# Kernel optimization log

Hardware: AMD Instinct MI355X
Metric: run time of the kernel (lower is better)

## Reference

```python
import jax, jax.numpy as jnp
import numpy as np

EMBED_DIM = 1024
N_HEADS = 16
HEAD_DIM = EMBED_DIM // N_HEADS


def setup_inputs() -> dict:
    key = jax.random.key(0)
    k1, k2, k3 = jax.random.split(key, 3)
    B, T, D = 2, 2048, EMBED_DIM
    x = jax.random.normal(k1, (B, T, D), dtype=jnp.float32)
    # torch nn.Linear weights: (out_features, in_features); y = x @ W.T
    scale = 1.0 / np.sqrt(D)
    qkv_w = jax.random.uniform(k2, (3 * D, D), dtype=jnp.float32, minval=-scale, maxval=scale)
    out_w = jax.random.uniform(k3, (D, D), dtype=jnp.float32, minval=-scale, maxval=scale)
    return {"x": x, "qkv_w": qkv_w, "out_w": out_w}


def reference(x, qkv_w, out_w):
    B, T, D = x.shape
    H, hd = N_HEADS, HEAD_DIM
    qkv = jnp.einsum('btd,ed->bte', x, qkv_w)  # (B,T,3D)
    qkv = qkv.reshape(B, T, 3, H, hd)
    q = jnp.transpose(qkv[:, :, 0], (0, 2, 1, 3))  # (B,H,T,hd)
    k = jnp.transpose(qkv[:, :, 1], (0, 2, 1, 3))
    v = jnp.transpose(qkv[:, :, 2], (0, 2, 1, 3))
    scores = jnp.einsum('bhtd,bhsd->bhts', q, k) / np.sqrt(hd).astype(np.float32)
    causal = jnp.tril(jnp.ones((T, T), dtype=bool))  # True = keep
    scores = jnp.where(causal[None, None], scores, -jnp.inf)
    probs = jax.nn.softmax(scores, axis=-1)
    out = jnp.einsum('bhts,bhsd->bhtd', probs, v)
    out = jnp.transpose(out, (0, 2, 1, 3)).reshape(B, T, D)
    return jnp.einsum('btd,ed->bte', out, out_w)
```

## Files before the change

### kernel.cpp

```cpp
#include <hip/hip_runtime.h>
#include <stdint.h>

typedef __bf16 bf16;
typedef __attribute__((ext_vector_type(8))) __bf16 bf16x8;
typedef __attribute__((ext_vector_type(4))) __bf16 bf16x4;
typedef __attribute__((ext_vector_type(4))) float f32x4;

#define AS1 __attribute__((address_space(1)))
#define AS3 __attribute__((address_space(3)))

__device__ __forceinline__ void async16(const void* g, void* l) {
  __builtin_amdgcn_global_load_lds((AS1 uint32_t*)(g), (AS3 uint32_t*)(l), 16, 0, 0);
}

__device__ __forceinline__ f32x4 mfma_bf16(bf16x8 a, bf16x8 b, f32x4 c) {
  return __builtin_amdgcn_mfma_f32_16x16x32_bf16(a, b, c, 0, 0, 0);
}

__device__ __forceinline__ uint32_t pack_bf16(float a, float b) {
  union { bf16 h[2]; uint32_t u; } u;
  u.h[0] = (bf16)a; u.h[1] = (bf16)b;
  return u.u;
}

__global__ __launch_bounds__(256) void cast_all_kernel(
    const float* __restrict__ x, const float* __restrict__ w1,
    const float* __restrict__ w2, bf16* __restrict__ xb,
    bf16* __restrict__ w1b, bf16* __restrict__ w2b) {
  const int bid = blockIdx.x;
  const float* src;
  bf16* dst;
  int base;
  if (bid < 4096) { src = x;  dst = xb;  base = bid; }
  else if (bid < 7168) { src = w1; dst = w1b; base = bid - 4096; }
  else { src = w2; dst = w2b; base = bid - 7168; }
  const int i = (base * 256 + threadIdx.x) * 4;
  const float4 v = *(const float4*)(src + i);
  bf16x4 o;
  o[0] = (bf16)v.x; o[1] = (bf16)v.y; o[2] = (bf16)v.z; o[3] = (bf16)v.w;
  *(bf16x4*)(dst + i) = o;
}

__global__ __launch_bounds__(256) void gemm_qkv_kernel(
    const bf16* __restrict__ A, const bf16* __restrict__ W,
    bf16* __restrict__ QK, bf16* __restrict__ VT) {
  constexpr int K = 1024;
  __shared__ __align__(16) bf16 sm[2 * 128 * 32];
  const int tid = threadIdx.x;
  const int w = tid >> 6, lane = tid & 63;
  const int m0 = blockIdx.x * 128, n0 = blockIdx.y * 128;
  const int wm = (w >> 1) * 64, wn = (w & 1) * 64;
  const int lrow = lane & 15, quad = lane >> 4;
  const int lk = quad * 8;
  f32x4 acc[4][4] = {};

  for (int k0 = 0; k0 < K; k0 += 32) {
#pragma unroll
    for (int i = 0; i < 4; ++i) {
      const int c = tid + 256 * i;
      const bf16* src = (c < 512)
          ? (A + (size_t)(m0 + (c >> 2)) * K + k0 + (c & 3) * 8)
          : (W + (size_t)(n0 + ((c - 512) >> 2)) * K + k0 + (c & 3) * 8);
      async16(src, sm + (w * 64 + i * 256) * 8);
    }
    __syncthreads();
    bf16x8 af[4], bfr[4];
#pragma unroll
    for (int mi = 0; mi < 4; ++mi)
      af[mi] = *(const bf16x8*)&sm[(wm + mi * 16 + lrow) * 32 + lk];
#pragma unroll
    for (int ni = 0; ni < 4; ++ni)
      bfr[ni] = *(const bf16x8*)&sm[128 * 32 + (wn + ni * 16 + lrow) * 32 + lk];
#pragma unroll
    for (int mi = 0; mi < 4; ++mi)
#pragma unroll
      for (int ni = 0; ni < 4; ++ni)
        acc[mi][ni] = mfma_bf16(af[mi], bfr[ni], acc[mi][ni]);
    __syncthreads();
  }

  bf16* s2 = sm;
  const bool isV = (n0 >= 2048);
  const int bb = m0 >> 11;
  const int mt = m0 & 2047;
  if (!isV) {
#pragma unroll
    for (int c = 0; c < 2; ++c) {
      if ((w >> 1) == c) {
#pragma unroll
        for (int mi = 0; mi < 4; ++mi)
#pragma unroll
          for (int ni = 0; ni < 4; ++ni) {
            const int nr = wn + ni * 16 + lrow;
#pragma unroll
            for (int r = 0; r < 4; ++r)
              s2[(mi * 16 + quad * 4 + r) * 128 + nr] = (bf16)acc[mi][ni][r];
          }
      }
      __syncthreads();
#pragma unroll
      for (int p = 0; p < 4; ++p) {
        const int row = p * 16 + (tid >> 4);
        const int colc = (tid & 15) * 8;
        const bf16x8 v = *(const bf16x8*)&s2[row * 128 + colc];
        *(bf16x8*)(QK + (size_t)(m0 + c * 64 + row) * 2048 + n0 + colc) = v;
      }
      __syncthreads();
    }
  } else {
#pragma unroll
    for (int c = 0; c < 2; ++c) {
      if ((w & 1) == c) {
#pragma unroll
        for (int mi = 0; mi < 4; ++mi)
#pragma unroll
          for (int ni = 0; ni < 4; ++ni) {
            const int nl = ni * 16 + lrow;
            bf16x4 pk4;
#pragma unroll
            for (int r = 0; r < 4; ++r) pk4[r] = (bf16)acc[mi][ni][r];
            *(bf16x4*)&s2[nl * 128 + wm + mi * 16 + quad * 4] = pk4;
          }
      }
      __syncthreads();
#pragma unroll
      for (int p = 0; p < 4; ++p) {
        const int row = p * 16 + (tid >> 4);
        const int colc = (tid & 15) * 8;
        const bf16x8 v = *(const bf16x8*)&s2[row * 128 + colc];
        const int vtrow = bb * 1024 + (n0 - 2048) + c * 64 + row;
        *(bf16x8*)(VT + (size_t)vtrow * 2048 + mt + colc) = v;
      }
      __syncthreads();
    }
  }
}

__global__ __launch_bounds__(128) void attn_kernel(
    const bf16* __restrict__ QK, const bf16* __restrict__ VT,
    bf16* __restrict__ AO) {
  __shared__ __align__(16) bf16 sK[2][64 * 64];
  __shared__ __align__(16) bf16 sV[2][64 * 64];
  const int bh = blockIdx.x;
  const int qt = 31 - blockIdx.y;
  const int b = bh >> 4, h = bh & 15;
  const int tid = threadIdx.x, w = tid >> 6, lane = tid & 63;
  const int q0 = qt * 64;
  const int col = lane & 15, quad = lane >> 4;
  const bf16* Qb = QK + (size_t)b * 2048 * 2048 + h * 64;
  const bf16* Kb = Qb + 1024;
  const bf16* Vb = VT + (size_t)bh * 64 * 2048;
  const float NEG_INF = -__builtin_inff();
  constexpr float QSCALE = 0.18033688011112042f;
  constexpr float FMX = 16.0f;

  int qrow[2];
  bf16x8 qf[2][2];
#pragma unroll
  for (int qtile = 0; qtile < 2; ++qtile) {
    qrow[qtile] = q0 + w * 32 + qtile * 16 + col;
#pragma unroll
    for (int kk = 0; kk < 2; ++kk) {
      bf16x8 v = *(const bf16x8*)(Qb + (size_t)qrow[qtile] * 2048 + kk * 32 + quad * 8);
#pragma unroll
      for (int e = 0; e < 8; ++e) v[e] = (bf16)((float)v[e] * QSCALE);
      qf[qtile][kk] = v;
    }
  }

  auto stage = [&](int buf, int s0) {
#pragma unroll
    for (int i = 0; i < 4; ++i) {
      const int L = tid + 128 * i;
      const int row = L >> 3;
      const int ch = (L & 7) ^ (row & 7);
      async16(Kb + (size_t)(s0 + row) * 2048 + ch * 8, &sK[buf][L * 8]);
    }
#pragma unroll
    for (int i = 0; i < 4; ++i) {
      const int L = tid + 128 * i;
      const int row = L >> 3;
      const int ch = (L & 7) ^ (row & 7);
      async16(Vb + (size_t)row * 2048 + s0 + ch * 8, &sV[buf][L * 8]);
    }
  };

  int srow[4];
#pragma unroll
  for (int m = 0; m < 4; ++m)
    srow[m] = 32 * (m & 1) + (col >> 2) * 8 + 4 * (m >> 1) + (col & 3);

  f32x4 accO[4][2] = {};
  float l_part[2] = {0.f, 0.f};

  stage(0, 0);

  auto body = [&](int kt, bool masked) {
    const int s0 = kt * 64;
    const bf16* kbuf = sK[kt & 1];
    const bf16* vbuf = sV[kt & 1];

    f32x4 st[2][4] = {};
#pragma unroll
    for (int kk = 0; kk < 2; ++kk) {
      bf16x8 kf[4];
#pragma unroll
      for (int m = 0; m < 4; ++m)
        kf[m] = *(const bf16x8*)&kbuf[srow[m] * 64 + (((kk * 4 + quad) ^ (srow[m] & 7)) * 8)];
#pragma unroll
      for (int m = 0; m < 4; ++m)
#pragma unroll
        for (int qtile = 0; qtile < 2; ++qtile)
          st[qtile][m] = mfma_bf16(kf[m], qf[qtile][kk], st[qtile][m]);
    }

    if (masked) {
#pragma unroll
      for (int qtile = 0; qtile < 2; ++qtile)
#pragma unroll
        for (int m = 0; m < 4; ++m) {
          const int kvb = s0 + 32 * (m & 1) + quad * 8 + 4 * (m >> 1);
#pragma unroll
          for (int r = 0; r < 4; ++r)
            st[qtile][m][r] = (kvb + r <= qrow[qtile]) ? st[qtile][m][r] : NEG_INF;
        }
    }

    uint32_t pk[2][4][2];
#pragma unroll
    for (int qtile = 0; qtile < 2; ++qtile) {
      float rs = 0.f;
#pragma unroll
      for (int m = 0; m < 4; ++m) {
        const float p0 = __builtin_amdgcn_exp2f(st[qtile][m][0] - FMX);
        const float p1 = __builtin_amdgcn_exp2f(st[qtile][m][1] - FMX);
        const float p2 = __builtin_amdgcn_exp2f(st[qtile][m][2] - FMX);
        const float p3 = __builtin_amdgcn_exp2f(st[qtile][m][3] - FMX);
        rs += (p0 + p1) + (p2 + p3);
        pk[qtile][m][0] = pack_bf16(p0, p1);
        pk[qtile][m][1] = pack_bf16(p2, p3);
      }
      l_part[qtile] += rs;
    }

#pragma unroll
    for (int kk = 0; kk < 2; ++kk) {
      bf16x8 vf[4];
#pragma unroll
      for (int d = 0; d < 4; ++d) {
        const int row = d * 16 + col;
        vf[d] = *(const bf16x8*)&vbuf[row * 64 + (((kk * 4 + quad) ^ (row & 7)) * 8)];
      }
#pragma unroll
      for (int qtile = 0; qtile < 2; ++qtile) {
        union { uint32_t u[4]; bf16x8 v; } f;
        f.u[0] = pk[qtile][kk][0];
        f.u[1] = pk[qtile][kk][1];
        f.u[2] = pk[qtile][2 + kk][0];
        f.u[3] = pk[qtile][2 + kk][1];
#pragma unroll
        for (int d = 0; d < 4; ++d)
          accO[d][qtile] = mfma_bf16(vf[d], f.v, accO[d][qtile]);
      }
    }
  };

  for (int kt = 0; kt < qt; ++kt) {
    __syncthreads();
    stage((kt + 1) & 1, (kt + 1) * 64);
    body(kt, false);
  }
  __syncthreads();
  body(qt, true);

  bf16* Ob = AO + (size_t)b * 2048 * 1024 + h * 64;
#pragma unroll
  for (int qtile = 0; qtile < 2; ++qtile) {
    float rs = l_part[qtile];
    rs += __shfl_xor(rs, 16);
    rs += __shfl_xor(rs, 32);
    const float inv = 1.0f / rs;
#pragma unroll
    for (int d = 0; d < 4; ++d) {
      bf16x4 o;
#pragma unroll
      for (int r = 0; r < 4; ++r) o[r] = (bf16)(accO[d][qtile][r] * inv);
      *(bf16x4*)(Ob + (size_t)qrow[qtile] * 1024 + d * 16 + quad * 4) = o;
    }
  }
}

__global__ __launch_bounds__(256) void gemm_out_kernel(
    const bf16* __restrict__ A, const bf16* __restrict__ W,
    float* __restrict__ C) {
  constexpr int K = 1024;
  __shared__ __align__(16) bf16 sm[2 * 128 * 32];
  const int tid = threadIdx.x;
  const int w = tid >> 6, lane = tid & 63;
  const int m0 = blockIdx.x * 128, n0 = blockIdx.y * 128;
  const int wm = (w >> 1) * 64, wn = (w & 1) * 64;
  const int lrow = lane & 15, lk = (lane >> 4) * 8;
  f32x4 acc[4][4] = {};

  for (int k0 = 0; k0 < K; k0 += 32) {
#pragma unroll
    for (int i = 0; i < 4; ++i) {
      const int c = tid + 256 * i;
      const bf16* src = (c < 512)
          ? (A + (size_t)(m0 + (c >> 2)) * K + k0 + (c & 3) * 8)
          : (W + (size_t)(n0 + ((c - 512) >> 2)) * K + k0 + (c & 3) * 8);
      async16(src, sm + (w * 64 + i * 256) * 8);
    }
    __syncthreads();
    bf16x8 af[4], bfr[4];
#pragma unroll
    for (int mi = 0; mi < 4; ++mi)
      af[mi] = *(const bf16x8*)&sm[(wm + mi * 16 + lrow) * 32 + lk];
#pragma unroll
    for (int ni = 0; ni < 4; ++ni)
      bfr[ni] = *(const bf16x8*)&sm[128 * 32 + (wn + ni * 16 + lrow) * 32 + lk];
#pragma unroll
    for (int mi = 0; mi < 4; ++mi)
#pragma unroll
      for (int ni = 0; ni < 4; ++ni)
        acc[mi][ni] = mfma_bf16(af[mi], bfr[ni], acc[mi][ni]);
    __syncthreads();
  }

#pragma unroll
  for (int mi = 0; mi < 4; ++mi)
#pragma unroll
    for (int ni = 0; ni < 4; ++ni) {
      const int n = n0 + wn + ni * 16 + lrow;
#pragma unroll
      for (int r = 0; r < 4; ++r) {
        const int m = m0 + wm + mi * 16 + (lane >> 4) * 4 + r;
        C[(size_t)m * 1024 + n] = acc[mi][ni][r];
      }
    }
}

extern "C" void kernel_launch(void* const* d_in, const int* in_sizes, int n_in,
                              void* d_out, int out_size, void* d_ws, size_t ws_size,
                              hipStream_t stream) {
  const float* x     = (const float*)d_in[0];
  const float* qkv_w = (const float*)d_in[1];
  const float* out_w = (const float*)d_in[2];
  float* out = (float*)d_out;

  char* ws = (char*)d_ws;
  bf16* xb    = (bf16*)(ws);
  bf16* aob   = (bf16*)(ws);
  bf16* wqkvb = (bf16*)(ws + 8u * 1024 * 1024);
  bf16* wob   = (bf16*)(ws + 14u * 1024 * 1024);
  bf16* qkb   = (bf16*)(ws + 16u * 1024 * 1024);
  bf16* vtb   = (bf16*)(ws + 32u * 1024 * 1024);

  cast_all_kernel<<<8192, 256, 0, stream>>>(x, qkv_w, out_w, xb, wqkvb, wob);
  gemm_qkv_kernel<<<dim3(32, 24), 256, 0, stream>>>(xb, wqkvb, qkb, vtb);
  attn_kernel<<<dim3(32, 32), 128, 0, stream>>>(qkb, vtb, aob);
  gemm_out_kernel<<<dim3(32, 8), 256, 0, stream>>>(aob, wob, out);
}
```

Baseline: 183.7 us.

## Split KV tiles across warp pairs in attention and reduce partials via LDS

Doubles attention block size to four warps. Each pair of warps handles the same query rows and takes alternate KV tiles, with both tiles staged into LDS together. Partial output accumulators and row sums are combined through shared memory before normalization. This raises per-block parallelism and shortens the serial KV loop, at the cost of losing prefetch/compute overlap and adding extra barriers and a final reduction.

```diff
diff --git a/kernel.cpp b/kernel.cpp
--- a/kernel.cpp
+++ b/kernel.cpp
@@ -136,7 +136,7 @@
   }
 }
 
-__global__ __launch_bounds__(128) void attn_kernel(
+__global__ __launch_bounds__(256) void attn_kernel(
     const bf16* __restrict__ QK, const bf16* __restrict__ VT,
     bf16* __restrict__ AO) {
   __shared__ __align__(16) bf16 sK[2][64 * 64];
@@ -145,6 +145,7 @@
   const int qt = 31 - blockIdx.y;
   const int b = bh >> 4, h = bh & 15;
   const int tid = threadIdx.x, w = tid >> 6, lane = tid & 63;
+  const int qhalf = w >> 1, parity = w & 1;
   const int q0 = qt * 64;
   const int col = lane & 15, quad = lane >> 4;
   const bf16* Qb = QK + (size_t)b * 2048 * 2048 + h * 64;
@@ -158,7 +159,7 @@
   bf16x8 qf[2][2];
 #pragma unroll
   for (int qtile = 0; qtile < 2; ++qtile) {
-    qrow[qtile] = q0 + w * 32 + qtile * 16 + col;
+    qrow[qtile] = q0 + qhalf * 32 + qtile * 16 + col;
 #pragma unroll
     for (int kk = 0; kk < 2; ++kk) {
       bf16x8 v = *(const bf16x8*)(Qb + (size_t)qrow[qtile] * 2048 + kk * 32 + quad * 8);
@@ -168,20 +169,22 @@
     }
   }
 
-  auto stage = [&](int buf, int s0) {
+  auto stage = [&](int s0) {
 #pragma unroll
     for (int i = 0; i < 4; ++i) {
-      const int L = tid + 128 * i;
-      const int row = L >> 3;
-      const int ch = (L & 7) ^ (row & 7);
-      async16(Kb + (size_t)(s0 + row) * 2048 + ch * 8, &sK[buf][L * 8]);
+      const int L = tid + 256 * i;
+      const int buf = L >> 9, Lr = L & 511;
+      const int row = Lr >> 3;
+      const int ch = (Lr & 7) ^ (row & 7);
+      async16(Kb + (size_t)(s0 + buf * 64 + row) * 2048 + ch * 8, &sK[0][L * 8]);
     }
 #pragma unroll
     for (int i = 0; i < 4; ++i) {
-      const int L = tid + 128 * i;
-      const int row = L >> 3;
-      const int ch = (L & 7) ^ (row & 7);
-      async16(Vb + (size_t)row * 2048 + s0 + ch * 8, &sV[buf][L * 8]);
+      const int L = tid + 256 * i;
+      const int buf = L >> 9, Lr = L & 511;
+      const int d = Lr >> 3;
+      const int ch = (Lr & 7) ^ (d & 7);
+      async16(Vb + (size_t)d * 2048 + s0 + buf * 64 + ch * 8, &sV[0][L * 8]);
     }
   };
 
@@ -193,12 +196,10 @@
   f32x4 accO[4][2] = {};
   float l_part[2] = {0.f, 0.f};
 
-  stage(0, 0);
-
   auto body = [&](int kt, bool masked) {
     const int s0 = kt * 64;
-    const bf16* kbuf = sK[kt & 1];
-    const bf16* vbuf = sV[kt & 1];
+    const bf16* kbuf = &sK[0][parity * 4096];
+    const bf16* vbuf = &sV[0][parity * 4096];
 
     f32x4 st[2][4] = {};
 #pragma unroll
@@ -265,27 +266,54 @@
     }
   };
 
-  for (int kt = 0; kt < qt; ++kt) {
-    __syncthreads();
-    stage((kt + 1) & 1, (kt + 1) * 64);
-    body(kt, false);
+  const int npairs = (qt >> 1) + 1;
+  for (int j = 0; j < npairs; ++j) {
+    stage(j * 128);
+    __syncthreads();
+    const int kt = 2 * j + parity;
+    if (kt <= qt) body(kt, kt == qt);
+    __syncthreads();
+  }
+
+  float* scrO = (float*)sK;
+  float* scrL = (float*)sV;
+  if (parity == 1) {
+    const int base = qhalf * 2048;
+#pragma unroll
+    for (int d = 0; d < 4; ++d)
+#pragma unroll
+      for (int qtile = 0; qtile < 2; ++qtile)
+#pragma unroll
+        for (int r = 0; r < 4; ++r)
+          scrO[base + ((d * 2 + qtile) * 4 + r) * 64 + lane] = accO[d][qtile][r];
+#pragma unroll
+    for (int qtile = 0; qtile < 2; ++qtile)
+      scrL[qhalf * 128 + qtile * 64 + lane] = l_part[qtile];
   }
   __syncthreads();
-  body(qt, true);
-
-  bf16* Ob = AO + (size_t)b * 2048 * 1024 + h * 64;
-#pragma unroll
-  for (int qtile = 0; qtile < 2; ++qtile) {
-    float rs = l_part[qtile];
-    rs += __shfl_xor(rs, 16);
-    rs += __shfl_xor(rs, 32);
-    const float inv = 1.0f / rs;
-#pragma unroll
-    for (int d = 0; d < 4; ++d) {
-      bf16x4 o;
-#pragma unroll
-      for (int r = 0; r < 4; ++r) o[r] = (bf16)(accO[d][qtile][r] * inv);
-      *(bf16x4*)(Ob + (size_t)qrow[qtile] * 1024 + d * 16 + quad * 4) = o;
+  if (parity == 0) {
+    const int base = qhalf * 2048;
+#pragma unroll
+    for (int d = 0; d < 4; ++d)
+#pragma unroll
+      for (int qtile = 0; qtile < 2; ++qtile)
+#pragma unroll
+        for (int r = 0; r < 4; ++r)
+          accO[d][qtile][r] += scrO[base + ((d * 2 + qtile) * 4 + r) * 64 + lane];
+    bf16* Ob = AO + (size_t)b * 2048 * 1024 + h * 64;
+#pragma unroll
+    for (int qtile = 0; qtile < 2; ++qtile) {
+      float rs = l_part[qtile] + scrL[qhalf * 128 + qtile * 64 + lane];
+      rs += __shfl_xor(rs, 16);
+      rs += __shfl_xor(rs, 32);
+      const float inv = 1.0f / rs;
+#pragma unroll
+      for (int d = 0; d < 4; ++d) {
+        bf16x4 o;
+#pragma unroll
+        for (int r = 0; r < 4; ++r) o[r] = (bf16)(accO[d][qtile][r] * inv);
+        *(bf16x4*)(Ob + (size_t)qrow[qtile] * 1024 + d * 16 + quad * 4) = o;
+      }
     }
   }
 }
@@ -358,6 +386,6 @@
 
   cast_all_kernel<<<8192, 256, 0, stream>>>(x, qkv_w, out_w, xb, wqkvb, wob);
   gemm_qkv_kernel<<<dim3(32, 24), 256, 0, stream>>>(xb, wqkvb, qkb, vtb);
-  attn_kernel<<<dim3(32, 32), 128, 0, stream>>>(qkb, vtb, aob);
+  attn_kernel<<<dim3(32, 32), 256, 0, stream>>>(qkb, vtb, aob);
   gemm_out_kernel<<<dim3(32, 8), 256, 0, stream>>>(aob, wob, out);
 }
```

Result: faster. 173.7 us (-5.5%).

## Drop LDS staging in attention; per-wave direct global loads with register prefetch

Applied to the files above, without the earlier changes.

The attention kernel stops staging K/V tiles through LDS with async copies and barriers. Each wave now handles its own 32-row query tile and reads K and V fragments straight from global memory into registers, prefetching the next K tile while the current one is computed. Causal work is trimmed per wave: a wave skips the second half of the last KV tile when the diagonal falls in the first half. The fixed exp2 offset subtraction is also removed. The change gets rid of block-wide syncs and LDS traffic, but relies on L1/L2 to catch K/V reuse across waves and may raise global-load latency exposure.

```diff
diff --git a/kernel.cpp b/kernel.cpp
--- a/kernel.cpp
+++ b/kernel.cpp
@@ -136,29 +136,120 @@
   }
 }
 
-__global__ __launch_bounds__(128) void attn_kernel(
+template <bool HALF, bool MASK>
+__device__ __forceinline__ void attn_body(
+    bf16x8 (&kf)[4][2], const bf16* Vt, const bf16* Kn,
+    const int* koff, const int* voff,
+    const bf16x8 (&qf)[2][2], f32x4 (&accO)[4][2], float (&l_part)[2],
+    int col, int quad) {
+  const float NEG_INF = -__builtin_inff();
+  bf16x8 vf[2][4];
+#pragma unroll
+  for (int kk = 0; kk < (HALF ? 1 : 2); ++kk)
+#pragma unroll
+    for (int d = 0; d < 4; ++d)
+      vf[kk][d] = *(const bf16x8*)(Vt + voff[d] + kk * 32);
+
+  f32x4 st[2][4];
+#pragma unroll
+  for (int qtile = 0; qtile < 2; ++qtile)
+#pragma unroll
+    for (int m = 0; m < 4; ++m)
+      st[qtile][m] = f32x4{0.f, 0.f, 0.f, 0.f};
+#pragma unroll
+  for (int kk = 0; kk < 2; ++kk)
+#pragma unroll
+    for (int m = 0; m < 4; ++m) {
+      if (HALF && (m & 1)) continue;
+#pragma unroll
+      for (int qtile = 0; qtile < 2; ++qtile)
+        st[qtile][m] = mfma_bf16(kf[m][kk], qf[qtile][kk], st[qtile][m]);
+    }
+
+  if (Kn) {
+#pragma unroll
+    for (int m = 0; m < 4; ++m)
+#pragma unroll
+      for (int kk = 0; kk < 2; ++kk)
+        kf[m][kk] = *(const bf16x8*)(Kn + koff[m] + kk * 32);
+  }
+
+  if (MASK) {
+#pragma unroll
+    for (int qtile = 0; qtile < 2; ++qtile) {
+      const int rq = qtile * 16 + col;
+#pragma unroll
+      for (int m = 0; m < 4; ++m) {
+        if (HALF ? ((m & 1) != 0) : ((m & 1) == 0)) continue;
+        const int kvb = quad * 8 + 4 * (m >> 1);
+#pragma unroll
+        for (int r = 0; r < 4; ++r)
+          st[qtile][m][r] = (kvb + r <= rq) ? st[qtile][m][r] : NEG_INF;
+      }
+    }
+  }
+
+  uint32_t pk[2][4][2];
+#pragma unroll
+  for (int qtile = 0; qtile < 2; ++qtile) {
+    float rs = 0.f;
+#pragma unroll
+    for (int m = 0; m < 4; ++m) {
+      if (HALF && (m & 1)) continue;
+      const float p0 = __builtin_amdgcn_exp2f(st[qtile][m][0]);
+      const float p1 = __builtin_amdgcn_exp2f(st[qtile][m][1]);
+      const float p2 = __builtin_amdgcn_exp2f(st[qtile][m][2]);
+      const float p3 = __builtin_amdgcn_exp2f(st[qtile][m][3]);
+      rs += (p0 + p1) + (p2 + p3);
+      pk[qtile][m][0] = pack_bf16(p0, p1);
+      pk[qtile][m][1] = pack_bf16(p2, p3);
+    }
+    l_part[qtile] += rs;
+  }
+
+#pragma unroll
+  for (int kk = 0; kk < (HALF ? 1 : 2); ++kk)
+#pragma unroll
+    for (int qtile = 0; qtile < 2; ++qtile) {
+      union { uint32_t u[4]; bf16x8 v; } f;
+      f.u[0] = pk[qtile][kk][0];
+      f.u[1] = pk[qtile][kk][1];
+      f.u[2] = pk[qtile][2 + kk][0];
+      f.u[3] = pk[qtile][2 + kk][1];
+#pragma unroll
+      for (int d = 0; d < 4; ++d)
+        accO[d][qtile] = mfma_bf16(vf[kk][d], f.v, accO[d][qtile]);
+    }
+}
+
+__global__ __launch_bounds__(256) void attn_kernel(
     const bf16* __restrict__ QK, const bf16* __restrict__ VT,
     bf16* __restrict__ AO) {
-  __shared__ __align__(16) bf16 sK[2][64 * 64];
-  __shared__ __align__(16) bf16 sV[2][64 * 64];
   const int bh = blockIdx.x;
-  const int qt = 31 - blockIdx.y;
   const int b = bh >> 4, h = bh & 15;
   const int tid = threadIdx.x, w = tid >> 6, lane = tid & 63;
-  const int q0 = qt * 64;
+  const int qt = 4 * (15 - (int)blockIdx.y) + w;
+  const int q0 = qt * 32;
   const int col = lane & 15, quad = lane >> 4;
   const bf16* Qb = QK + (size_t)b * 2048 * 2048 + h * 64;
   const bf16* Kb = Qb + 1024;
   const bf16* Vb = VT + (size_t)bh * 64 * 2048;
-  const float NEG_INF = -__builtin_inff();
   constexpr float QSCALE = 0.18033688011112042f;
-  constexpr float FMX = 16.0f;
+
+  int koff[4], voff[4];
+#pragma unroll
+  for (int m = 0; m < 4; ++m) {
+    const int sigma = 32 * (m & 1) + (col >> 2) * 8 + 4 * (m >> 1) + (col & 3);
+    koff[m] = sigma * 2048 + quad * 8;
+  }
+#pragma unroll
+  for (int d = 0; d < 4; ++d) voff[d] = (d * 16 + col) * 2048 + quad * 8;
 
   int qrow[2];
   bf16x8 qf[2][2];
 #pragma unroll
   for (int qtile = 0; qtile < 2; ++qtile) {
-    qrow[qtile] = q0 + w * 32 + qtile * 16 + col;
+    qrow[qtile] = q0 + qtile * 16 + col;
 #pragma unroll
     for (int kk = 0; kk < 2; ++kk) {
       bf16x8 v = *(const bf16x8*)(Qb + (size_t)qrow[qtile] * 2048 + kk * 32 + quad * 8);
@@ -168,110 +259,30 @@
     }
   }
 
-  auto stage = [&](int buf, int s0) {
-#pragma unroll
-    for (int i = 0; i < 4; ++i) {
-      const int L = tid + 128 * i;
-      const int row = L >> 3;
-      const int ch = (L & 7) ^ (row & 7);
-      async16(Kb + (size_t)(s0 + row) * 2048 + ch * 8, &sK[buf][L * 8]);
-    }
-#pragma unroll
-    for (int i = 0; i < 4; ++i) {
-      const int L = tid + 128 * i;
-      const int row = L >> 3;
-      const int ch = (L & 7) ^ (row & 7);
-      async16(Vb + (size_t)row * 2048 + s0 + ch * 8, &sV[buf][L * 8]);
-    }
-  };
-
-  int srow[4];
+  const bf16* Kt = Kb;
+  const bf16* Vt = Vb;
+  bf16x8 kf[4][2];
 #pragma unroll
   for (int m = 0; m < 4; ++m)
-    srow[m] = 32 * (m & 1) + (col >> 2) * 8 + 4 * (m >> 1) + (col & 3);
+#pragma unroll
+    for (int kk = 0; kk < 2; ++kk)
+      kf[m][kk] = *(const bf16x8*)(Kt + koff[m] + kk * 32);
 
   f32x4 accO[4][2] = {};
   float l_part[2] = {0.f, 0.f};
 
-  stage(0, 0);
-
-  auto body = [&](int kt, bool masked) {
-    const int s0 = kt * 64;
-    const bf16* kbuf = sK[kt & 1];
-    const bf16* vbuf = sV[kt & 1];
-
-    f32x4 st[2][4] = {};
-#pragma unroll
-    for (int kk = 0; kk < 2; ++kk) {
-      bf16x8 kf[4];
-#pragma unroll
-      for (int m = 0; m < 4; ++m)
-        kf[m] = *(const bf16x8*)&kbuf[srow[m] * 64 + (((kk * 4 + quad) ^ (srow[m] & 7)) * 8)];
-#pragma unroll
-      for (int m = 0; m < 4; ++m)
-#pragma unroll
-        for (int qtile = 0; qtile < 2; ++qtile)
-          st[qtile][m] = mfma_bf16(kf[m], qf[qtile][kk], st[qtile][m]);
-    }
-
-    if (masked) {
-#pragma unroll
-      for (int qtile = 0; qtile < 2; ++qtile)
-#pragma unroll
-        for (int m = 0; m < 4; ++m) {
-          const int kvb = s0 + 32 * (m & 1) + quad * 8 + 4 * (m >> 1);
-#pragma unroll
-          for (int r = 0; r < 4; ++r)
-            st[qtile][m][r] = (kvb + r <= qrow[qtile]) ? st[qtile][m][r] : NEG_INF;
-        }
-    }
-
-    uint32_t pk[2][4][2];
-#pragma unroll
-    for (int qtile = 0; qtile < 2; ++qtile) {
-      float rs = 0.f;
-#pragma unroll
-      for (int m = 0; m < 4; ++m) {
-        const float p0 = __builtin_amdgcn_exp2f(st[qtile][m][0] - FMX);
-        const float p1 = __builtin_amdgcn_exp2f(st[qtile][m][1] - FMX);
-        const float p2 = __builtin_amdgcn_exp2f(st[qtile][m][2] - FMX);
-        const float p3 = __builtin_amdgcn_exp2f(st[qtile][m][3] - FMX);
-        rs += (p0 + p1) + (p2 + p3);
-        pk[qtile][m][0] = pack_bf16(p0, p1);
-        pk[qtile][m][1] = pack_bf16(p2, p3);
-      }
-      l_part[qtile] += rs;
-    }
-
-#pragma unroll
-    for (int kk = 0; kk < 2; ++kk) {
-      bf16x8 vf[4];
-#pragma unroll
-      for (int d = 0; d < 4; ++d) {
-        const int row = d * 16 + col;
-        vf[d] = *(const bf16x8*)&vbuf[row * 64 + (((kk * 4 + quad) ^ (row & 7)) * 8)];
-      }
-#pragma unroll
-      for (int qtile = 0; qtile < 2; ++qtile) {
-        union { uint32_t u[4]; bf16x8 v; } f;
-        f.u[0] = pk[qtile][kk][0];
-        f.u[1] = pk[qtile][kk][1];
-        f.u[2] = pk[qtile][2 + kk][0];
-        f.u[3] = pk[qtile][2 + kk][1];
-#pragma unroll
-        for (int d = 0; d < 4; ++d)
-          accO[d][qtile] = mfma_bf16(vf[d], f.v, accO[d][qtile]);
-      }
-    }
-  };
-
-  for (int kt = 0; kt < qt; ++kt) {
-    __syncthreads();
-    stage((kt + 1) & 1, (kt + 1) * 64);
-    body(kt, false);
-  }
-  __syncthreads();
-  body(qt, true);
+  const int nt = (qt >> 1) + 1;
+#pragma unroll 1
+  for (int t = 0; t < nt - 1; ++t) {
+    const bf16* Kn = Kt + 64 * 2048;
+    attn_body<false, false>(kf, Vt, Kn, koff, voff, qf, accO, l_part, col, quad);
+    Kt = Kn;
+    Vt += 64;
+  }
+  if (qt & 1)
+    attn_body<false, true>(kf, Vt, nullptr, koff, voff, qf, accO, l_part, col, quad);
+  else
+    attn_body<true, true>(kf, Vt, nullptr, koff, voff, qf, accO, l_part, col, quad);
 
   bf16* Ob = AO + (size_t)b * 2048 * 1024 + h * 64;
 #pragma unroll
@@ -358,6 +369,6 @@
 
   cast_all_kernel<<<8192, 256, 0, stream>>>(x, qkv_w, out_w, xb, wqkvb, wob);
   gemm_qkv_kernel<<<dim3(32, 24), 256, 0, stream>>>(xb, wqkvb, qkb, vtb);
-  attn_kernel<<<dim3(32, 32), 128, 0, stream>>>(qkb, vtb, aob);
+  attn_kernel<<<dim3(32, 16), 256, 0, stream>>>(qkb, vtb, aob);
   gemm_out_kernel<<<dim3(32, 8), 256, 0, stream>>>(aob, wob, out);
 }
```

Measured after the change: 221.4 us. 20.5% more time.
